# Kernel tuning notes

Hardware: AMD Instinct MI355X
Metric: run time of the kernel (lower is better)

## Reference

```python
import math
import jax, jax.numpy as jnp
import numpy as np

B, H, I, O = 8192, 2048, 1024, 512
EPS = 1e-6
T_INF = 10000.0


def next_spike(v, eta):
    sqrt_eta = jnp.sqrt(jnp.abs(eta) + EPS)
    v_safe = v + EPS * jnp.sign(v) + 0.5 * EPS * jnp.sign(v + EPS)
    pi = jnp.asarray(math.pi, v.dtype)
    case_zero = jnp.where(v > 0, 1.0 / v_safe, T_INF)
    case_neg = jnp.where(
        v > sqrt_eta,
        jnp.arctanh(jnp.clip(sqrt_eta / v_safe, -1 + EPS, 1 - EPS)) / sqrt_eta,
        T_INF,
    )
    case_pos = jnp.mod(jnp.arctan(sqrt_eta / v_safe), pi) / sqrt_eta
    return jnp.where(eta == 0, case_zero, jnp.where(eta < 0, case_neg, case_pos))


def update_potential(v, eta, dt):
    sqrt_eta = jnp.sqrt(jnp.abs(eta) + EPS)
    th = jnp.tanh(sqrt_eta * dt)
    ta = jnp.tan(sqrt_eta * dt)
    case_zero = v / (1 - dt * v)
    case_neg = (v - sqrt_eta * th) / (1 - th * v / sqrt_eta)
    case_pos = (v + sqrt_eta * ta) / (1 - ta * v / sqrt_eta)
    v_new = jnp.where(eta == 0, case_zero, jnp.where(eta < 0, case_neg, case_pos))
    return jnp.clip(v_new, -1e25, 1e25)


def setup_inputs():
    key = jax.random.key(0)
    ks = jax.random.split(key, 10)
    return dict(
        input_spike=jax.random.normal(ks[0], (B, H), jnp.float32) * 0.1,
        input_current=jax.random.normal(ks[1], (B, I), jnp.float32),
        v=jax.random.normal(ks[2], (B, H), jnp.float32),
        t=jnp.zeros((B,), jnp.float32),
        w_i2h=jax.random.normal(ks[3], (H, I), jnp.float32) / math.sqrt(I),
        b_i2h=jax.random.normal(ks[4], (H,), jnp.float32) / math.sqrt(I),
        w_h2h=jax.random.normal(ks[5], (H, H), jnp.float32) / math.sqrt(H),
        b_h2h=jax.random.normal(ks[6], (H,), jnp.float32),
        w_h2o=jax.random.normal(ks[7], (O, H), jnp.float32) / math.sqrt(H),
        b_h2o=jax.random.normal(ks[8], (O,), jnp.float32) / math.sqrt(H),
        syn_delay=jnp.float32(0.1),
        vmin=jnp.float32(-10.0),
        vmax=jnp.float32(10.0),
    )


def reference(input_spike, input_current, v, t, w_i2h, b_i2h, w_h2h, b_h2h,
              w_h2o, b_h2o, syn_delay, vmin, vmax):
    # v <- v + spikes; eta = h2h.bias + i2h(current)
    v = v + input_spike                                   # [B,H]
    eta = b_h2h + input_current @ w_i2h.T + b_i2h         # [B,H]
    dt_all = next_spike(v, eta)                           # [B,H]
    min_dt = jnp.min(dt_all, axis=1)                      # [B]
    k = jnp.argmin(dt_all, axis=1)                        # [B] int
    v = update_potential(v, eta, (min_dt + syn_delay)[:, None])
    v = v + jnp.take(w_h2h.T, k, axis=0)                  # recurrent column gather
    t = t + min_dt + syn_delay
    output_spike = jnp.take(w_h2o.T, k, axis=0)           # [B,O]
    output_potential = jnp.clip(v, vmin, vmax) @ w_h2o.T + b_h2o  # [B,O]
    return (output_spike, output_potential, v, t, min_dt, k)
```

## Files before the change

### kernel.cpp

```cpp
#include <hip/hip_runtime.h>
#include <math.h>

#define B_SZ 8192
#define H_SZ 2048
#define I_SZ 1024
#define O_SZ 512

typedef double v4d __attribute__((ext_vector_type(4)));


__device__ __forceinline__ float signf_(float x) {
    return (x > 0.f) ? 1.f : ((x < 0.f) ? -1.f : 0.f);
}

__device__ __forceinline__ float next_spike_f32(float v, float eta) {
#pragma clang fp contract(off)
    const float EPSf = 1e-6f;
    const float HEPSf = (float)(0.5 * 1e-6);
    const float T_INF = 10000.f;
    const float PI_F = (float)3.14159265358979323846;
    float ae = fabsf(eta) + EPSf;
    float se = (float)sqrt((double)ae);
    float s1 = signf_(v);
    float t1 = EPSf * s1;
    float va = v + t1;
    float vpe = v + EPSf;
    float s2 = signf_(vpe);
    float t2 = HEPSf * s2;
    float vs = va + t2;
    if (eta == 0.f) {
        if (v > 0.f) return 1.f / vs;
        return T_INF;
    }
    if (eta < 0.f) {
        if (v > se) {
            float r = se / vs;
            const float lo = (float)(-1.0 + 1e-6);
            const float hi = (float)(1.0 - 1e-6);
            r = fminf(fmaxf(r, lo), hi);
            float at = atanhf(r);
            return at / se;
        }
        return T_INF;
    }
    float q = se / vs;
    float a = atanf(q);
    if (a < 0.f) a = a + PI_F;
    return a / se;
}

__device__ __forceinline__ float update_pot_f32(float v, float eta, float dt) {
#pragma clang fp contract(off)
    const float EPSf = 1e-6f;
    float ae = fabsf(eta) + EPSf;
    float se = (float)sqrt((double)ae);
    float r;
    if (eta == 0.f) {
        float t1 = dt * v;
        float den = 1.f - t1;
        r = v / den;
    } else if (eta < 0.f) {
        float x = se * dt;
        float th = tanhf(x);
        float t1 = se * th;
        float num = v - t1;
        float t2 = th * v;
        float t3 = t2 / se;
        float den = 1.f - t3;
        r = num / den;
    } else {
        float x = se * dt;
        float ta = tanf(x);
        float t1 = se * ta;
        float num = v + t1;
        float t2 = ta * v;
        float t3 = t2 / se;
        float den = 1.f - t3;
        r = num / den;
    }
    const float HI = (float)1e25;
    r = r < -HI ? -HI : (r > HI ? HI : r);
    return r;
}


__global__ __launch_bounds__(256) void transpose_kernel(const float* __restrict__ in,
                                                        float* __restrict__ out,
                                                        int R, int C) {
    __shared__ float tile[32][33];
    int bx = blockIdx.x * 32;
    int by = blockIdx.y * 32;
    int tx = threadIdx.x;
    int ty = threadIdx.y;
#pragma unroll
    for (int i = ty; i < 32; i += 8)
        tile[i][tx] = in[(size_t)(by + i) * C + bx + tx];
    __syncthreads();
#pragma unroll
    for (int i = ty; i < 32; i += 8)
        out[(size_t)(bx + i) * R + by + tx] = tile[tx][i];
}


#define EBK 32

__device__ __forceinline__ void stage_tile_dma(
    const float* __restrict__ A, const float* __restrict__ Bm,
    float (*Asb)[32], float (*Bsb)[32],
    int row0, int col0, int k0, int tid) {
    const int wid = tid >> 6;
    const int lane = tid & 63;
    const int sr8 = lane >> 3;
    const int ksw = ((lane & 7) ^ sr8) << 2;
#pragma unroll
    for (int p = 0; p < 2; ++p) {
        const int rbase = p * 64 + wid * 8;
        const float* ga = A + (size_t)(row0 + rbase + sr8) * I_SZ + k0 + ksw;
        const float* gb = Bm + (size_t)(col0 + rbase + sr8) * I_SZ + k0 + ksw;
        float* la = &Asb[rbase][0];
        float* lb = &Bsb[rbase][0];
        __builtin_amdgcn_global_load_lds(
            (const __attribute__((address_space(1))) void*)ga,
            (__attribute__((address_space(3))) void*)la, 16, 0, 0);
        __builtin_amdgcn_global_load_lds(
            (const __attribute__((address_space(1))) void*)gb,
            (__attribute__((address_space(3))) void*)lb, 16, 0, 0);
    }
}

__global__ __launch_bounds__(512) void gemm_eta_mfma_f64(
    const float* __restrict__ A,
    const float* __restrict__ Bm,
    const float* __restrict__ b_i2h, const float* __restrict__ b_h2h,
    float* __restrict__ C) {
    __shared__ float As[2][128][32];
    __shared__ float Bs[2][128][32];
    const int tid = threadIdx.x;
    const int row0 = blockIdx.y * 128;
    const int col0 = blockIdx.x * 128;
    const int wid = tid >> 6;
    const int lane = tid & 63;
    const int wrow = wid >> 1;
    const int wcol = wid & 1;
    const int lr = lane & 15;
    const int lk = lane >> 4;
    const int csw = (lr & 7) << 2;

    v4d acc[2][4];
#pragma unroll
    for (int i = 0; i < 2; ++i)
#pragma unroll
        for (int j = 0; j < 4; ++j) acc[i][j] = (v4d){0.0, 0.0, 0.0, 0.0};

    stage_tile_dma(A, Bm, As[0], Bs[0], row0, col0, 0, tid);
    __syncthreads();

    int cur = 0;
    for (int k0 = 0; k0 < I_SZ; k0 += EBK) {
        int knext = k0 + EBK;
        if (knext < I_SZ)
            stage_tile_dma(A, Bm, As[cur ^ 1], Bs[cur ^ 1], row0, col0, knext, tid);
#pragma unroll
        for (int ks = 0; ks < EBK / 4; ++ks) {
            int kk = ks * 4 + lk;
            int kks = kk ^ csw;
            double a[2], b[4];
#pragma unroll
            for (int i = 0; i < 2; ++i)
                a[i] = (double)As[cur][wrow * 32 + i * 16 + lr][kks];
#pragma unroll
            for (int j = 0; j < 4; ++j)
                b[j] = (double)Bs[cur][wcol * 64 + j * 16 + lr][kks];
#pragma unroll
            for (int i = 0; i < 2; ++i)
#pragma unroll
                for (int j = 0; j < 4; ++j)
                    acc[i][j] = __builtin_amdgcn_mfma_f64_16x16x4f64(
                        a[i], b[j], acc[i][j], 0, 0, 0);
        }
        __syncthreads();
        cur ^= 1;
    }
    {
#pragma clang fp contract(off)
#pragma unroll
        for (int i = 0; i < 2; ++i) {
#pragma unroll
            for (int j = 0; j < 4; ++j) {
                int gcol = col0 + wcol * 64 + j * 16 + lr;
#pragma unroll
                for (int q = 0; q < 4; ++q) {
                    int grow = row0 + wrow * 32 + i * 16 + q * 4 + lk;
                    float m32 = (float)acc[i][j][q];
                    float s = b_h2h[gcol] + m32;
                    s = s + b_i2h[gcol];
                    C[(size_t)grow * H_SZ + gcol] = s;
                }
            }
        }
    }
}


__global__ __launch_bounds__(256) void spike_min_kernel(
    const float* __restrict__ v_in, const float* __restrict__ spike,
    const float* __restrict__ eta, const float* __restrict__ t_in,
    const float* __restrict__ syn_p,
    float* __restrict__ t_out, float* __restrict__ mdt_out,
    float* __restrict__ kf_out, int* __restrict__ kidx) {
#pragma clang fp contract(off)
    const int b = blockIdx.x;
    const int tid = threadIdx.x;
    const size_t base = (size_t)b * H_SZ;
    unsigned long long best = 0xFFFFFFFFFFFFFFFFull;
    for (int h = tid; h < H_SZ; h += 256) {
        float vv = v_in[base + h] + spike[base + h];
        float dt = next_spike_f32(vv, eta[base + h]);
        unsigned long long p =
            ((unsigned long long)__float_as_uint(dt) << 32) | (unsigned)h;
        best = (p < best) ? p : best;
    }
#pragma unroll
    for (int off = 1; off < 64; off <<= 1) {
        unsigned long long o = __shfl_xor(best, off);
        best = (o < best) ? o : best;
    }
    __shared__ unsigned long long s[4];
    if ((tid & 63) == 0) s[tid >> 6] = best;
    __syncthreads();
    if (tid == 0) {
        best = s[0];
#pragma unroll
        for (int w = 1; w < 4; ++w)
            if (s[w] < best) best = s[w];
        float mdt = __uint_as_float((unsigned)(best >> 32));
        int k = (int)(best & 0xFFFFFFFFu);
        mdt_out[b] = mdt;
        kf_out[b] = (float)k;
        kidx[b] = k;
        float tt = t_in[b] + mdt;
        tt = tt + (*syn_p);
        t_out[b] = tt;
    }
}


__global__ __launch_bounds__(256) void update_v_kernel(
    const float* __restrict__ v_in, const float* __restrict__ spike,
    const float* __restrict__ eta, const float* __restrict__ mdt,
    const int* __restrict__ kidx, const float* __restrict__ whhT,
    const float* __restrict__ syn_p, float* __restrict__ v_out) {
#pragma clang fp contract(off)
    size_t i4 = ((size_t)blockIdx.x * 256 + threadIdx.x) * 4;
    if (i4 >= (size_t)B_SZ * H_SZ) return;
    int b = (int)(i4 >> 11);
    int h = (int)(i4 & (H_SZ - 1));
    float dt = mdt[b] + (*syn_p);
    int k = kidx[b];
    float4 v4 = *reinterpret_cast<const float4*>(v_in + i4);
    float4 s4 = *reinterpret_cast<const float4*>(spike + i4);
    float4 e4 = *reinterpret_cast<const float4*>(eta + i4);
    float4 w4 = *reinterpret_cast<const float4*>(whhT + (size_t)k * H_SZ + h);
    float4 r;
    r.x = update_pot_f32(v4.x + s4.x, e4.x, dt) + w4.x;
    r.y = update_pot_f32(v4.y + s4.y, e4.y, dt) + w4.y;
    r.z = update_pot_f32(v4.z + s4.z, e4.z, dt) + w4.z;
    r.w = update_pot_f32(v4.w + s4.w, e4.w, dt) + w4.w;
    *reinterpret_cast<float4*>(v_out + i4) = r;
}


__global__ __launch_bounds__(256) void out_spike_kernel(
    const int* __restrict__ kidx, const float* __restrict__ whoT,
    float* __restrict__ out0) {
    size_t i4 = ((size_t)blockIdx.x * 256 + threadIdx.x) * 4;
    if (i4 >= (size_t)B_SZ * O_SZ) return;
    int b = (int)(i4 >> 9);
    int o = (int)(i4 & (O_SZ - 1));
    int k = kidx[b];
    float4 w = *reinterpret_cast<const float4*>(whoT + (size_t)k * O_SZ + o);
    *reinterpret_cast<float4*>(out0 + i4) = w;
}


#define GT 128
#define GK 16

__global__ __launch_bounds__(256, 2) void gemm_f32_clip_kernel(
    const float* __restrict__ A, const float* __restrict__ Bm,
    const float* __restrict__ bias0, float* __restrict__ C,
    int K, const float* __restrict__ vminp, const float* __restrict__ vmaxp) {
    __shared__ float As[GK][GT + 4];
    __shared__ float Bs[GK][GT + 4];
    const int tid = threadIdx.x;
    const int row0 = blockIdx.y * GT;
    const int col0 = blockIdx.x * GT;
    const float vmin = *vminp, vmax = *vmaxp;
    const int lr = tid >> 2;
    const int lc = (tid & 3) << 2;
    const int ty = tid >> 4;
    const int tx = tid & 15;

    float acc[8][8];
#pragma unroll
    for (int i = 0; i < 8; ++i)
#pragma unroll
        for (int j = 0; j < 8; ++j) acc[i][j] = 0.f;

    for (int k0 = 0; k0 < K; k0 += GK) {
#pragma unroll
        for (int half = 0; half < 2; ++half) {
            int r = lr + half * 64;
            float4 a4 = *reinterpret_cast<const float4*>(A + (size_t)(row0 + r) * K + k0 + lc);
            a4.x = fminf(fmaxf(a4.x, vmin), vmax);
            a4.y = fminf(fmaxf(a4.y, vmin), vmax);
            a4.z = fminf(fmaxf(a4.z, vmin), vmax);
            a4.w = fminf(fmaxf(a4.w, vmin), vmax);
            As[lc + 0][r] = a4.x; As[lc + 1][r] = a4.y;
            As[lc + 2][r] = a4.z; As[lc + 3][r] = a4.w;
            float4 b4 = *reinterpret_cast<const float4*>(Bm + (size_t)(col0 + r) * K + k0 + lc);
            Bs[lc + 0][r] = b4.x; Bs[lc + 1][r] = b4.y;
            Bs[lc + 2][r] = b4.z; Bs[lc + 3][r] = b4.w;
        }
        __syncthreads();
#pragma unroll
        for (int kk = 0; kk < GK; ++kk) {
            float a[8], b[8];
#pragma unroll
            for (int i = 0; i < 8; ++i) a[i] = As[kk][ty * 8 + i];
#pragma unroll
            for (int j = 0; j < 8; ++j) b[j] = Bs[kk][tx * 8 + j];
#pragma unroll
            for (int i = 0; i < 8; ++i)
#pragma unroll
                for (int j = 0; j < 8; ++j) acc[i][j] = fmaf(a[i], b[j], acc[i][j]);
        }
        __syncthreads();
    }

    float bb[8];
#pragma unroll
    for (int j = 0; j < 8; ++j) bb[j] = bias0[col0 + tx * 8 + j];
#pragma unroll
    for (int i = 0; i < 8; ++i) {
        int row = row0 + ty * 8 + i;
#pragma unroll
        for (int j = 0; j < 8; j += 4) {
            float4 vstore;
            vstore.x = acc[i][j + 0] + bb[j + 0];
            vstore.y = acc[i][j + 1] + bb[j + 1];
            vstore.z = acc[i][j + 2] + bb[j + 2];
            vstore.w = acc[i][j + 3] + bb[j + 3];
            *reinterpret_cast<float4*>(C + (size_t)row * O_SZ + col0 + tx * 8 + j) = vstore;
        }
    }
}


extern "C" void kernel_launch(void* const* d_in, const int* in_sizes, int n_in,
                              void* d_out, int out_size, void* d_ws, size_t ws_size,
                              hipStream_t stream) {
    const float* in_spike = (const float*)d_in[0];
    const float* in_cur   = (const float*)d_in[1];
    const float* v_in     = (const float*)d_in[2];
    const float* t_in     = (const float*)d_in[3];
    const float* w_i2h    = (const float*)d_in[4];
    const float* b_i2h    = (const float*)d_in[5];
    const float* w_h2h    = (const float*)d_in[6];
    const float* b_h2h    = (const float*)d_in[7];
    const float* w_h2o    = (const float*)d_in[8];
    const float* b_h2o    = (const float*)d_in[9];
    const float* syn_p    = (const float*)d_in[10];
    const float* vmin_p   = (const float*)d_in[11];
    const float* vmax_p   = (const float*)d_in[12];

    float* out0    = (float*)d_out;
    float* out1    = out0 + (size_t)B_SZ * O_SZ;
    float* out_v   = out1 + (size_t)B_SZ * O_SZ;
    float* out_t   = out_v + (size_t)B_SZ * H_SZ;
    float* out_mdt = out_t + B_SZ;
    float* out_kf  = out_mdt + B_SZ;

    float* eta  = (float*)d_ws;
    int*   kidx = (int*)(eta + (size_t)B_SZ * H_SZ);
    float* whhT = (float*)(kidx + B_SZ);
    float* whoT = whhT + (size_t)H_SZ * H_SZ;

    dim3 tb(32, 8);
    transpose_kernel<<<dim3(H_SZ / 32, H_SZ / 32), tb, 0, stream>>>(w_h2h, whhT,
                                                                    H_SZ, H_SZ);
    transpose_kernel<<<dim3(H_SZ / 32, O_SZ / 32), tb, 0, stream>>>(w_h2o, whoT,
                                                                    O_SZ, H_SZ);

    gemm_eta_mfma_f64<<<dim3(H_SZ / 128, B_SZ / 128), 512, 0, stream>>>(
        in_cur, w_i2h, b_i2h, b_h2h, eta);

    spike_min_kernel<<<B_SZ, 256, 0, stream>>>(v_in, in_spike, eta, t_in, syn_p,
                                               out_t, out_mdt, out_kf, kidx);

    update_v_kernel<<<(B_SZ * H_SZ / 4 + 255) / 256, 256, 0, stream>>>(
        v_in, in_spike, eta, out_mdt, kidx, whhT, syn_p, out_v);

    out_spike_kernel<<<(B_SZ * O_SZ / 4 + 255) / 256, 256, 0, stream>>>(kidx, whoT,
                                                                        out0);

    gemm_f32_clip_kernel<<<dim3(O_SZ / GT, B_SZ / GT), 256, 0, stream>>>(
        out_v, w_h2o, b_h2o, out1, H_SZ, vmin_p, vmax_p);
}
```

Baseline: 942.5 us.

## Replace FP32 output GEMM with split-bf16 three-pass MFMA GEMM

The clipped output projection GEMM moves from scalar FP32 FMAs with 128x128 tiles to bf16 MFMA instructions. Each operand is split into a high and a low bf16 part, and three MFMA products (hh, hl, lh) approximate FP32 accuracy. This trades scalar ALU throughput for matrix-core throughput. It adds per-tile conversion work, uses smaller 64x64 tiles with more global reloads, writes output with scalar uncoalesced stores, and carries a slight accuracy risk.

New measurement: 789.6 us. -16.2%, faster.

```diff
diff --git a/kernel.cpp b/kernel.cpp
--- a/kernel.cpp
+++ b/kernel.cpp
@@ -7,6 +7,8 @@
 #define O_SZ 512
 
 typedef double v4d __attribute__((ext_vector_type(4)));
+typedef float v4f __attribute__((ext_vector_type(4)));
+typedef short v8bf __attribute__((ext_vector_type(8)));
 
 
 __device__ __forceinline__ float signf_(float x) {
@@ -283,77 +285,100 @@
 }
 
 
-#define GT 128
-#define GK 16
-
-__global__ __launch_bounds__(256, 2) void gemm_f32_clip_kernel(
-    const float* __restrict__ A, const float* __restrict__ Bm,
+#define OBK 32
+
+__device__ __forceinline__ unsigned short bf16_rn(float x) {
+    unsigned u = __float_as_uint(x);
+    unsigned r = (u + 0x7fffu + ((u >> 16) & 1u)) >> 16;
+    return (unsigned short)r;
+}
+
+__global__ __launch_bounds__(256) void gemm_out1_bf16x3(
+    const float* __restrict__ A,
+    const float* __restrict__ Bm,
     const float* __restrict__ bias0, float* __restrict__ C,
-    int K, const float* __restrict__ vminp, const float* __restrict__ vmaxp) {
-    __shared__ float As[GK][GT + 4];
-    __shared__ float Bs[GK][GT + 4];
+    const float* __restrict__ vminp, const float* __restrict__ vmaxp) {
+    __shared__ unsigned short Ah[64][40], Al[64][40];
+    __shared__ unsigned short Bh[64][40], Bl[64][40];
     const int tid = threadIdx.x;
-    const int row0 = blockIdx.y * GT;
-    const int col0 = blockIdx.x * GT;
+    const int row0 = blockIdx.y * 64;
+    const int col0 = blockIdx.x * 64;
     const float vmin = *vminp, vmax = *vmaxp;
-    const int lr = tid >> 2;
-    const int lc = (tid & 3) << 2;
-    const int ty = tid >> 4;
-    const int tx = tid & 15;
-
-    float acc[8][8];
-#pragma unroll
-    for (int i = 0; i < 8; ++i)
-#pragma unroll
-        for (int j = 0; j < 8; ++j) acc[i][j] = 0.f;
-
-    for (int k0 = 0; k0 < K; k0 += GK) {
-#pragma unroll
-        for (int half = 0; half < 2; ++half) {
-            int r = lr + half * 64;
-            float4 a4 = *reinterpret_cast<const float4*>(A + (size_t)(row0 + r) * K + k0 + lc);
-            a4.x = fminf(fmaxf(a4.x, vmin), vmax);
-            a4.y = fminf(fmaxf(a4.y, vmin), vmax);
-            a4.z = fminf(fmaxf(a4.z, vmin), vmax);
-            a4.w = fminf(fmaxf(a4.w, vmin), vmax);
-            As[lc + 0][r] = a4.x; As[lc + 1][r] = a4.y;
-            As[lc + 2][r] = a4.z; As[lc + 3][r] = a4.w;
-            float4 b4 = *reinterpret_cast<const float4*>(Bm + (size_t)(col0 + r) * K + k0 + lc);
-            Bs[lc + 0][r] = b4.x; Bs[lc + 1][r] = b4.y;
-            Bs[lc + 2][r] = b4.z; Bs[lc + 3][r] = b4.w;
+    const int wid = tid >> 6, lane = tid & 63;
+    const int wrow = wid >> 1, wcol = wid & 1;
+    const int lr = lane & 15;
+    const int lg = lane >> 4;
+    const int srow = tid >> 2;
+    const int scol = (tid & 3) * 8;
+
+    v4f acc[2][2];
+#pragma unroll
+    for (int i = 0; i < 2; ++i)
+#pragma unroll
+        for (int j = 0; j < 2; ++j) acc[i][j] = (v4f){0.f, 0.f, 0.f, 0.f};
+
+    for (int k0 = 0; k0 < H_SZ; k0 += OBK) {
+#pragma unroll
+        for (int p = 0; p < 2; ++p) {
+            float4 a4 = *reinterpret_cast<const float4*>(
+                A + (size_t)(row0 + srow) * H_SZ + k0 + scol + p * 4);
+            float4 b4 = *reinterpret_cast<const float4*>(
+                Bm + (size_t)(col0 + srow) * H_SZ + k0 + scol + p * 4);
+            float av[4] = {fminf(fmaxf(a4.x, vmin), vmax),
+                           fminf(fmaxf(a4.y, vmin), vmax),
+                           fminf(fmaxf(a4.z, vmin), vmax),
+                           fminf(fmaxf(a4.w, vmin), vmax)};
+            float bv[4] = {b4.x, b4.y, b4.z, b4.w};
+#pragma unroll
+            for (int e = 0; e < 4; ++e) {
+                int cc = scol + p * 4 + e;
+                unsigned short ha = bf16_rn(av[e]);
+                float hfa = __uint_as_float((unsigned)ha << 16);
+                Ah[srow][cc] = ha;
+                Al[srow][cc] = bf16_rn(av[e] - hfa);
+                unsigned short hb = bf16_rn(bv[e]);
+                float hfb = __uint_as_float((unsigned)hb << 16);
+                Bh[srow][cc] = hb;
+                Bl[srow][cc] = bf16_rn(bv[e] - hfb);
+            }
         }
         __syncthreads();
-#pragma unroll
-        for (int kk = 0; kk < GK; ++kk) {
-            float a[8], b[8];
-#pragma unroll
-            for (int i = 0; i < 8; ++i) a[i] = As[kk][ty * 8 + i];
-#pragma unroll
-            for (int j = 0; j < 8; ++j) b[j] = Bs[kk][tx * 8 + j];
-#pragma unroll
-            for (int i = 0; i < 8; ++i)
-#pragma unroll
-                for (int j = 0; j < 8; ++j) acc[i][j] = fmaf(a[i], b[j], acc[i][j]);
-        }
+        v8bf ah[2], al[2], bh[2], bl[2];
+#pragma unroll
+        for (int i = 0; i < 2; ++i) {
+            ah[i] = *reinterpret_cast<const v8bf*>(&Ah[wrow * 32 + i * 16 + lr][lg * 8]);
+            al[i] = *reinterpret_cast<const v8bf*>(&Al[wrow * 32 + i * 16 + lr][lg * 8]);
+        }
+#pragma unroll
+        for (int j = 0; j < 2; ++j) {
+            bh[j] = *reinterpret_cast<const v8bf*>(&Bh[wcol * 32 + j * 16 + lr][lg * 8]);
+            bl[j] = *reinterpret_cast<const v8bf*>(&Bl[wcol * 32 + j * 16 + lr][lg * 8]);
+        }
+#pragma unroll
+        for (int i = 0; i < 2; ++i)
+#pragma unroll
+            for (int j = 0; j < 2; ++j) {
+                acc[i][j] = __builtin_amdgcn_mfma_f32_16x16x32_bf16(
+                    ah[i], bh[j], acc[i][j], 0, 0, 0);
+                acc[i][j] = __builtin_amdgcn_mfma_f32_16x16x32_bf16(
+                    ah[i], bl[j], acc[i][j], 0, 0, 0);
+                acc[i][j] = __builtin_amdgcn_mfma_f32_16x16x32_bf16(
+                    al[i], bh[j], acc[i][j], 0, 0, 0);
+            }
         __syncthreads();
     }
-
-    float bb[8];
-#pragma unroll
-    for (int j = 0; j < 8; ++j) bb[j] = bias0[col0 + tx * 8 + j];
-#pragma unroll
-    for (int i = 0; i < 8; ++i) {
-        int row = row0 + ty * 8 + i;
-#pragma unroll
-        for (int j = 0; j < 8; j += 4) {
-            float4 vstore;
-            vstore.x = acc[i][j + 0] + bb[j + 0];
-            vstore.y = acc[i][j + 1] + bb[j + 1];
-            vstore.z = acc[i][j + 2] + bb[j + 2];
-            vstore.w = acc[i][j + 3] + bb[j + 3];
-            *reinterpret_cast<float4*>(C + (size_t)row * O_SZ + col0 + tx * 8 + j) = vstore;
-        }
-    }
+#pragma unroll
+    for (int i = 0; i < 2; ++i)
+#pragma unroll
+        for (int j = 0; j < 2; ++j) {
+            int gcol = col0 + wcol * 32 + j * 16 + lr;
+            float bb = bias0[gcol];
+#pragma unroll
+            for (int q = 0; q < 4; ++q) {
+                int grow = row0 + wrow * 32 + i * 16 + lg * 4 + q;
+                C[(size_t)grow * O_SZ + gcol] = acc[i][j][q] + bb;
+            }
+        }
 }
 
 
@@ -404,6 +429,6 @@
     out_spike_kernel<<<(B_SZ * O_SZ / 4 + 255) / 256, 256, 0, stream>>>(kidx, whoT,
                                                                         out0);
 
-    gemm_f32_clip_kernel<<<dim3(O_SZ / GT, B_SZ / GT), 256, 0, stream>>>(
-        out_v, w_h2o, b_h2o, out1, H_SZ, vmin_p, vmax_p);
-}
+    gemm_out1_bf16x3<<<dim3(O_SZ / 64, B_SZ / 64), 256, 0, stream>>>(
+        out_v, w_h2o, b_h2o, out1, vmin_p, vmax_p);
+}
```
